# Kernel tuning notes

Measured on AMD Instinct MI355X. Metric: run time of the kernel, lower is better.

## Reference

```python
import jax, jax.numpy as jnp
import numpy as np

KH, KW, STRIDE, PAD, DIL = 3, 3, 1, 1, 1


def setup_inputs() -> dict:
    key = jax.random.key(0)
    k1, k2, k3, k4, k5 = jax.random.split(key, 5)
    B, Cin, H, W = 8, 64, 128, 128
    Cout = 64
    K = KH * KW
    Ho = (H + 2 * PAD - DIL * (KH - 1) - 1) // STRIDE + 1
    Wo = (W + 2 * PAD - DIL * (KW - 1) - 1) // STRIDE + 1
    return {
        "input": jax.random.normal(k1, (B, Cin, H, W), dtype=jnp.float32),
        "offset": jax.random.normal(k2, (B, 2 * K, Ho, Wo), dtype=jnp.float32),
        "mask": jax.random.uniform(k3, (B, K, Ho, Wo), dtype=jnp.float32),
        "weight": jax.random.normal(k4, (Cout, Cin, KH, KW), dtype=jnp.float32) * 0.05,
        "bias": jax.random.normal(k5, (Cout,), dtype=jnp.float32) * 0.01,
    }


def _bilinear_gather(xb, py, px):
    # xb: [C,H,W]; py/px: [K,Ho,Wo] fractional sample coords. Zero padding outside.
    C, H, W = xb.shape
    y0 = jnp.floor(py)
    x0 = jnp.floor(px)
    wy = py - y0
    wx = px - x0

    def g(yi, xi):
        yi = yi.astype(jnp.int32)
        xi = xi.astype(jnp.int32)
        valid = ((yi >= 0) & (yi < H) & (xi >= 0) & (xi < W)).astype(xb.dtype)
        yc = jnp.clip(yi, 0, H - 1)
        xc = jnp.clip(xi, 0, W - 1)
        return xb[:, yc, xc] * valid[None]  # [C,K,Ho,Wo]

    return (g(y0, x0) * ((1 - wy) * (1 - wx))[None]
            + g(y0, x0 + 1) * ((1 - wy) * wx)[None]
            + g(y0 + 1, x0) * (wy * (1 - wx))[None]
            + g(y0 + 1, x0 + 1) * (wy * wx)[None])


def _deform_conv2d(x, offset, mask, weight, bias):
    B, Cin, H, W = x.shape
    Cout = weight.shape[0]
    K = KH * KW
    _, _, Ho, Wo = mask.shape
    # base sampling grid per kernel tap
    kh = jnp.arange(KH)
    kw = jnp.arange(KW)
    base_y = (jnp.arange(Ho) * STRIDE - PAD)[None, :] + (kh * DIL)[:, None]  # [KH,Ho]
    base_x = (jnp.arange(Wo) * STRIDE - PAD)[None, :] + (kw * DIL)[:, None]  # [KW,Wo]
    base_y = jnp.repeat(base_y, KW, axis=0)              # [K,Ho]
    base_x = jnp.tile(base_x, (KH, 1))                   # [K,Wo]
    off = offset.reshape(B, K, 2, Ho, Wo)                # torchvision layout: (y,x) per tap
    py = base_y[None, :, :, None].astype(x.dtype) + off[:, :, 0]  # [B,K,Ho,Wo]
    px = base_x[None, :, None, :].astype(x.dtype) + off[:, :, 1]
    sampled = jax.vmap(_bilinear_gather)(x, py, px)      # [B,Cin,K,Ho,Wo]
    sampled = sampled * mask[:, None]                    # modulated (DCNv2)
    w = weight.reshape(Cout, Cin, K)
    out = jnp.einsum('bckhw,ock->bohw', sampled, w) + bias[None, :, None, None]
    return out


def reference(input, offset, mask, weight, bias):
    out = _deform_conv2d(input, offset, mask, weight, bias)
    return jnp.clip(out, 0.0, 6.0)  # ReLU6
```

## Files before the change

### kernel.cpp

```cpp
#include <hip/hip_runtime.h>

typedef __attribute__((ext_vector_type(8))) short short8;
typedef __attribute__((ext_vector_type(8))) unsigned short ushort8;
typedef __attribute__((ext_vector_type(4))) float floatx4;
typedef __attribute__((ext_vector_type(4))) unsigned int uintx4;

constexpr int B = 8, Cin = 64, Hh = 128, Ww = 128, Cout = 64, Kt = 9, Ho = 128, Wo = 128;

__device__ __forceinline__ unsigned short f2bf(float f) {
    unsigned int u = __float_as_uint(f);
    unsigned int r = (u + 0x7fffu + ((u >> 16) & 1u)) >> 16;
    return (unsigned short)r;
}

__device__ __forceinline__ unsigned int cvtpk(float lo, float hi) {
    unsigned int r;
    asm("v_cvt_pk_bf16_f32 %0, %1, %2" : "=v"(r) : "v"(lo), "v"(hi));
    return r;
}
__device__ __forceinline__ float dot2bf(unsigned int a, unsigned int b, float c) {
    float d;
    asm("v_dot2_f32_bf16 %0, %1, %2, %3" : "=v"(d) : "v"(a), "v"(b), "v"(c));
    return d;
}

__global__ void prep_w(const float* __restrict__ w, unsigned short* __restrict__ wA) {
    int i = blockIdx.x * 256 + threadIdx.x;
    if (i >= Cout * Cin * Kt) return;
    int o = i / (Cin * Kt);
    int r = i % (Cin * Kt);
    int c = r / Kt;
    int k = r % Kt;
    wA[o * 576 + k * 64 + c] = f2bf(w[i]);
}

__global__ __launch_bounds__(256) void to_nhwc(const float* __restrict__ in,
                                               unsigned short* __restrict__ xn) {
    __shared__ float s[64 * 65];
    const int t = threadIdx.x;
    const int blk = blockIdx.x;
    const int b = blk >> 8;
    const int y = (blk & 255) >> 1;
    const int x0 = (blk & 1) * 64;
    const float* src = in + ((size_t)(b * 64) * 128 + y) * 128 + x0;
    #pragma unroll
    for (int i = 0; i < 16; ++i) {
        int c = i * 4 + (t >> 6);
        s[c * 65 + (t & 63)] = src[(size_t)c * 16384 + (t & 63)];
    }
    __syncthreads();
    const int x = t >> 2, c0 = (t & 3) * 16;
    ushort8 o0, o1;
    #pragma unroll
    for (int j = 0; j < 8; ++j) {
        o0[j] = f2bf(s[(c0 + j) * 65 + x]);
        o1[j] = f2bf(s[(c0 + 8 + j) * 65 + x]);
    }
    unsigned short* dst = xn + (((size_t)(b * 128 + y) * 128 + x0 + x) * 64 + c0);
    *(ushort8*)dst = o0;
    *(ushort8*)(dst + 8) = o1;
}

__global__ __launch_bounds__(256) void dcn_mfma(
    const unsigned short* __restrict__ xn, const float* __restrict__ off,
    const float* __restrict__ msk, const unsigned short* __restrict__ wA,
    const float* __restrict__ bias, float* __restrict__ out) {
    __shared__ uintx4 s_meta[Kt * 64];
    __shared__ unsigned short s_b[64 * 64];

    const int t = threadIdx.x;
    int blk = blockIdx.x;
    blk = (blk & 7) * 256 + (blk >> 3);
    const int b = blk >> 8;
    const int ho = (blk & 255) >> 1;
    const int w0 = (blk & 1) * 64;

    const int wv = t >> 6;
    const int l = t & 63;
    const int p = t >> 2;
    const int cg = t & 3;

    for (int idx = t; idx < Kt * 64; idx += 256) {
        const int k = idx >> 6, pp = idx & 63;
        const int kh = k / 3, kw = k - kh * 3;
        const int wo = w0 + pp;
        const size_t obase = ((size_t)b * 18 + 2 * k) * 16384 + ho * 128 + wo;
        const float oy = off[obase];
        const float ox = off[obase + 16384];
        const float m = msk[((size_t)b * 9 + k) * 16384 + ho * 128 + wo];
        const float py = (float)(ho - 1 + kh) + oy;
        const float px = (float)(wo - 1 + kw) + ox;
        const float y0f = floorf(py), x0f = floorf(px);
        const int iy0 = (int)y0f, ix0 = (int)x0f;
        const float wy = py - y0f, wx = px - x0f;
        const int iy1 = iy0 + 1, ix1 = ix0 + 1;
        const bool vy0 = ((unsigned)iy0 < 128u), vy1 = ((unsigned)iy1 < 128u);
        const bool vx0 = ((unsigned)ix0 < 128u), vx1 = ((unsigned)ix1 < 128u);
        const float w00 = (1.f - wy) * (1.f - wx) * m * ((vy0 && vx0) ? 1.f : 0.f);
        const float w01 = (1.f - wy) * wx * m * ((vy0 && vx1) ? 1.f : 0.f);
        const float w10 = wy * (1.f - wx) * m * ((vy1 && vx0) ? 1.f : 0.f);
        const float w11 = wy * wx * m * ((vy1 && vx1) ? 1.f : 0.f);
        const int cy0 = min(max(iy0, 0), 127), cy1 = min(max(iy1, 0), 127);
        const int cx0 = min(max(ix0, 0), 127), cx1 = min(max(ix1, 0), 127);
        const unsigned o00 = (unsigned)(cy0 * 128 + cx0), o01 = (unsigned)(cy0 * 128 + cx1);
        const unsigned o10 = (unsigned)(cy1 * 128 + cx0), o11 = (unsigned)(cy1 * 128 + cx1);
        uintx4 mt;
        mt.x = cvtpk(w00, w01);
        mt.y = cvtpk(w10, w11);
        mt.z = o00 | (o01 << 16);
        mt.w = o10 | (o11 << 16);
        s_meta[idx] = mt;
    }
    __syncthreads();

    floatx4 acc[4] = {};

    const unsigned short* wbase = wA + (16 * wv + (l & 15)) * 576 + (l >> 4) * 8;
    const unsigned short* xb = xn + (size_t)b * (128 * 128 * 64) + cg * 16;
    const int ckA = (cg * 2) ^ (p & 7);
    const int ckB = (cg * 2 + 1) ^ (p & 7);
    unsigned short* wrA = &s_b[p * 64 + ckA * 8];
    unsigned short* wrB = &s_b[p * 64 + ckB * 8];
    int rdo[8];
    #pragma unroll
    for (int h = 0; h < 2; ++h)
        #pragma unroll
        for (int f = 0; f < 4; ++f) {
            const int pp = 16 * f + (l & 15);
            const int ck = (h * 4 + (l >> 4)) ^ (pp & 7);
            rdo[h * 4 + f] = pp * 64 + ck * 8;
        }

    for (int k = 0; k < Kt; ++k) {
        const short8 a0 = *(const short8*)(wbase + k * 64);
        const short8 a1 = *(const short8*)(wbase + k * 64 + 32);

        const uintx4 mt = s_meta[k * 64 + p];
        const unsigned wp01 = mt.x, wp23 = mt.y;
        const uintx4* c00 = (const uintx4*)(xb + ((size_t)(mt.z & 0xffffu) << 6));
        const uintx4* c01 = (const uintx4*)(xb + ((size_t)(mt.z >> 16) << 6));
        const uintx4* c10 = (const uintx4*)(xb + ((size_t)(mt.w & 0xffffu) << 6));
        const uintx4* c11 = (const uintx4*)(xb + ((size_t)(mt.w >> 16) << 6));
        const uintx4 q00a = c00[0], q00b = c00[1];
        const uintx4 q01a = c01[0], q01b = c01[1];
        const uintx4 q10a = c10[0], q10b = c10[1];
        const uintx4 q11a = c11[0], q11b = c11[1];

        uintx4 vA, vB;
        #pragma unroll
        for (int j = 0; j < 4; ++j) {
            const unsigned pa = __builtin_amdgcn_perm(q01a[j], q00a[j], 0x05040100u);
            const unsigned pb = __builtin_amdgcn_perm(q11a[j], q10a[j], 0x05040100u);
            const unsigned pc = __builtin_amdgcn_perm(q01a[j], q00a[j], 0x07060302u);
            const unsigned pd = __builtin_amdgcn_perm(q11a[j], q10a[j], 0x07060302u);
            const float f0 = dot2bf(pa, wp01, dot2bf(pb, wp23, 0.f));
            const float f1 = dot2bf(pc, wp01, dot2bf(pd, wp23, 0.f));
            vA[j] = cvtpk(f0, f1);
        }
        #pragma unroll
        for (int j = 0; j < 4; ++j) {
            const unsigned pa = __builtin_amdgcn_perm(q01b[j], q00b[j], 0x05040100u);
            const unsigned pb = __builtin_amdgcn_perm(q11b[j], q10b[j], 0x05040100u);
            const unsigned pc = __builtin_amdgcn_perm(q01b[j], q00b[j], 0x07060302u);
            const unsigned pd = __builtin_amdgcn_perm(q11b[j], q10b[j], 0x07060302u);
            const float f0 = dot2bf(pa, wp01, dot2bf(pb, wp23, 0.f));
            const float f1 = dot2bf(pc, wp01, dot2bf(pd, wp23, 0.f));
            vB[j] = cvtpk(f0, f1);
        }
        *(uintx4*)wrA = vA;
        *(uintx4*)wrB = vB;
        __syncthreads();

        #pragma unroll
        for (int h = 0; h < 2; ++h) {
            const short8 a = h ? a1 : a0;
            #pragma unroll
            for (int f = 0; f < 4; ++f) {
                const short8 bfrag = *(const short8*)&s_b[rdo[h * 4 + f]];
                acc[f] = __builtin_amdgcn_mfma_f32_16x16x32_bf16(a, bfrag, acc[f], 0, 0, 0);
            }
        }
        __syncthreads();
    }

    #pragma unroll
    for (int f = 0; f < 4; ++f) {
        #pragma unroll
        for (int r = 0; r < 4; ++r) {
            const int co = 16 * wv + (l >> 4) * 4 + r;
            float v = acc[f][r] + bias[co];
            v = fminf(fmaxf(v, 0.f), 6.f);
            out[(((size_t)b * 64 + co) * 128 + ho) * 128 + w0 + 16 * f + (l & 15)] = v;
        }
    }
}

constexpr int NT = 64;
constexpr int LDSS = 68;

__global__ void reorder_weight(const float* __restrict__ w, float* __restrict__ wT) {
    int i = blockIdx.x * blockDim.x + threadIdx.x;
    if (i >= Cout * Cin * Kt) return;
    int o = i / (Cin * Kt);
    int r = i % (Cin * Kt);
    int c = r / Kt;
    int k = r % Kt;
    wT[(k * Cin + c) * Cout + o] = w[i];
}

__global__ __launch_bounds__(256, 4) void dcn_kernel(
    const float* __restrict__ in, const float* __restrict__ off,
    const float* __restrict__ msk, const float* __restrict__ wT,
    const float* __restrict__ bias, float* __restrict__ out) {
    __shared__ float s_w[Cin * LDSS];
    __shared__ float s_s[Cin * LDSS];
    const int tid = threadIdx.x;
    const int blk = blockIdx.x;
    const int b = blk >> 8;
    const int ho = (blk & 255) >> 1;
    const int w0 = (blk & 1) * NT;
    const int lane = tid & 63;
    const int c4 = tid >> 6;
    const int ty = tid >> 4;
    const int tx = tid & 15;
    const float* in_b = in + b * (Cin * Hh * Ww);
    const int wo = w0 + lane;
    float acc[4][4];
    #pragma unroll
    for (int i = 0; i < 4; ++i)
        #pragma unroll
        for (int j = 0; j < 4; ++j) acc[i][j] = 0.f;
    for (int k = 0; k < Kt; ++k) {
        {
            const float* src = wT + k * (Cin * Cout);
            const int c = tid >> 2;
            const int g = tid & 3;
            const float4* s = (const float4*)(src + c * Cout + g * 16);
            float4* dq = (float4*)(&s_w[c * LDSS + g * 16]);
            dq[0] = s[0]; dq[1] = s[1]; dq[2] = s[2]; dq[3] = s[3];
        }
        {
            const int kh = k / 3, kw = k % 3;
            const float oy = off[(((size_t)b * 2 * Kt + 2 * k) * Ho + ho) * Wo + wo];
            const float ox = off[(((size_t)b * 2 * Kt + 2 * k + 1) * Ho + ho) * Wo + wo];
            const float m = msk[(((size_t)b * Kt + k) * Ho + ho) * Wo + wo];
            const float py = (float)(ho - 1 + kh) + oy;
            const float px = (float)(wo - 1 + kw) + ox;
            const float y0f = floorf(py), x0f = floorf(px);
            const int iy0 = (int)y0f, ix0 = (int)x0f;
            const float wy = py - y0f, wx = px - x0f;
            const int iy1 = iy0 + 1, ix1 = ix0 + 1;
            const bool vy0 = (iy0 >= 0) & (iy0 < Hh);
            const bool vy1 = (iy1 >= 0) & (iy1 < Hh);
            const bool vx0 = (ix0 >= 0) & (ix0 < Ww);
            const bool vx1 = (ix1 >= 0) & (ix1 < Ww);
            const int cy0 = min(max(iy0, 0), Hh - 1), cy1 = min(max(iy1, 0), Hh - 1);
            const int cx0 = min(max(ix0, 0), Ww - 1), cx1 = min(max(ix1, 0), Ww - 1);
            const float w00 = (1.f - wy) * (1.f - wx) * m * ((vy0 & vx0) ? 1.f : 0.f);
            const float w01 = (1.f - wy) * wx * m * ((vy0 & vx1) ? 1.f : 0.f);
            const float w10 = wy * (1.f - wx) * m * ((vy1 & vx0) ? 1.f : 0.f);
            const float w11 = wy * wx * m * ((vy1 & vx1) ? 1.f : 0.f);
            const int o00 = cy0 * Ww + cx0, o01 = cy0 * Ww + cx1;
            const int o10 = cy1 * Ww + cx0, o11 = cy1 * Ww + cx1;
            const float* pp = in_b + (c4 * 16) * (Hh * Ww);
            #pragma unroll
            for (int ii = 0; ii < 16; ++ii) {
                float v = pp[o00] * w00 + pp[o01] * w01 + pp[o10] * w10 + pp[o11] * w11;
                s_s[(c4 * 16 + ii) * LDSS + lane] = v;
                pp += Hh * Ww;
            }
        }
        __syncthreads();
        #pragma unroll 8
        for (int c = 0; c < Cin; ++c) {
            const float4 a = *(const float4*)(&s_w[c * LDSS + ty * 4]);
            const float4 bv = *(const float4*)(&s_s[c * LDSS + tx * 4]);
            const float* ap = (const float*)&a;
            const float* bp = (const float*)&bv;
            #pragma unroll
            for (int i = 0; i < 4; ++i)
                #pragma unroll
                for (int j = 0; j < 4; ++j) acc[i][j] += ap[i] * bp[j];
        }
        __syncthreads();
    }
    #pragma unroll
    for (int i = 0; i < 4; ++i) {
        const int co = ty * 4 + i;
        const float bs = bias[co];
        float4 r;
        float* rp = (float*)&r;
        #pragma unroll
        for (int j = 0; j < 4; ++j) {
            float v = acc[i][j] + bs;
            v = fminf(fmaxf(v, 0.f), 6.f);
            rp[j] = v;
        }
        *(float4*)(&out[(((size_t)b * Cout + co) * Ho + ho) * Wo + w0 + tx * 4]) = r;
    }
}

extern "C" void kernel_launch(void* const* d_in, const int* in_sizes, int n_in,
                              void* d_out, int out_size, void* d_ws, size_t ws_size,
                              hipStream_t stream) {
    const float* in = (const float*)d_in[0];
    const float* off = (const float*)d_in[1];
    const float* msk = (const float*)d_in[2];
    const float* w = (const float*)d_in[3];
    const float* bias = (const float*)d_in[4];
    float* out = (float*)d_out;

    const size_t needX = (size_t)8 * 128 * 128 * 64 * 2;
    const size_t xoff = 131072;
    if (ws_size >= xoff + needX) {
        unsigned short* wAb = (unsigned short*)d_ws;
        unsigned short* xnb = (unsigned short*)((char*)d_ws + xoff);
        prep_w<<<144, 256, 0, stream>>>(w, wAb);
        to_nhwc<<<2048, 256, 0, stream>>>(in, xnb);
        dcn_mfma<<<2048, 256, 0, stream>>>(xnb, off, msk, wAb, bias, out);
    } else {
        float* wT = (float*)d_ws;
        reorder_weight<<<(Cout * Cin * Kt + 255) / 256, 256, 0, stream>>>(w, wT);
        dcn_kernel<<<(B * Ho * Wo) / NT, 256, 0, stream>>>(in, off, msk, wT, bias, out);
    }
}
```

Measured before the change: 61.14 us.

## Process two taps per iteration with double-buffered LDS to batch gathers

The tap loop now issues the bilinear gathers for two kernel taps back to back, blends both into two separate LDS buffers, then runs the MFMAs for both taps after a single barrier. This halves the number of barrier pairs and puts more global loads in flight at once, hiding gather latency. Address math is also switched to 32-bit byte offsets. The cost is roughly doubled live gather registers, which may lower occupancy, plus a larger LDS footprint.

```diff
diff --git a/kernel.cpp b/kernel.cpp
--- a/kernel.cpp
+++ b/kernel.cpp
@@ -12,7 +12,6 @@
     unsigned int r = (u + 0x7fffu + ((u >> 16) & 1u)) >> 16;
     return (unsigned short)r;
 }
-
 __device__ __forceinline__ unsigned int cvtpk(float lo, float hi) {
     unsigned int r;
     asm("v_cvt_pk_bf16_f32 %0, %1, %2" : "=v"(r) : "v"(lo), "v"(hi));
@@ -61,12 +60,17 @@
     *(ushort8*)(dst + 8) = o1;
 }
 
+struct Gath {
+    uintx4 q0, q1, q2, q3, q4, q5, q6, q7;
+    unsigned wp01, wp23;
+};
+
 __global__ __launch_bounds__(256) void dcn_mfma(
     const unsigned short* __restrict__ xn, const float* __restrict__ off,
     const float* __restrict__ msk, const unsigned short* __restrict__ wA,
     const float* __restrict__ bias, float* __restrict__ out) {
     __shared__ uintx4 s_meta[Kt * 64];
-    __shared__ unsigned short s_b[64 * 64];
+    __shared__ unsigned short s_b[2][64 * 64];
 
     const int t = threadIdx.x;
     int blk = blockIdx.x;
@@ -111,16 +115,16 @@
         mt.w = o10 | (o11 << 16);
         s_meta[idx] = mt;
     }
-    __syncthreads();
 
     floatx4 acc[4] = {};
 
     const unsigned short* wbase = wA + (16 * wv + (l & 15)) * 576 + (l >> 4) * 8;
-    const unsigned short* xb = xn + (size_t)b * (128 * 128 * 64) + cg * 16;
+    const char* xbase = (const char*)(xn + (size_t)b * (128 * 128 * 64));
+    const unsigned cgb = (unsigned)cg * 32u;
     const int ckA = (cg * 2) ^ (p & 7);
     const int ckB = (cg * 2 + 1) ^ (p & 7);
-    unsigned short* wrA = &s_b[p * 64 + ckA * 8];
-    unsigned short* wrB = &s_b[p * 64 + ckB * 8];
+    const int wrA = p * 64 + ckA * 8;
+    const int wrB = p * 64 + ckB * 8;
     int rdo[8];
     #pragma unroll
     for (int h = 0; h < 2; ++h)
@@ -131,56 +135,78 @@
             rdo[h * 4 + f] = pp * 64 + ck * 8;
         }
 
-    for (int k = 0; k < Kt; ++k) {
+    __syncthreads();
+
+    auto issue = [&](int k) -> Gath {
+        Gath g;
+        const uintx4 mt = s_meta[k * 64 + p];
+        g.wp01 = mt.x;
+        g.wp23 = mt.y;
+        const unsigned f00 = ((mt.z & 0xffffu) << 7) + cgb;
+        const unsigned f01 = ((mt.z >> 16) << 7) + cgb;
+        const unsigned f10 = ((mt.w & 0xffffu) << 7) + cgb;
+        const unsigned f11 = ((mt.w >> 16) << 7) + cgb;
+        const uintx4* c00 = (const uintx4*)(xbase + f00);
+        const uintx4* c01 = (const uintx4*)(xbase + f01);
+        const uintx4* c10 = (const uintx4*)(xbase + f10);
+        const uintx4* c11 = (const uintx4*)(xbase + f11);
+        g.q0 = c00[0]; g.q1 = c00[1];
+        g.q2 = c01[0]; g.q3 = c01[1];
+        g.q4 = c10[0]; g.q5 = c10[1];
+        g.q6 = c11[0]; g.q7 = c11[1];
+        return g;
+    };
+    auto blend_write = [&](int slot, const Gath& g) {
+        uintx4 vA, vB;
+        #pragma unroll
+        for (int j = 0; j < 4; ++j) {
+            const unsigned pa = __builtin_amdgcn_perm(g.q2[j], g.q0[j], 0x05040100u);
+            const unsigned pb = __builtin_amdgcn_perm(g.q6[j], g.q4[j], 0x05040100u);
+            const unsigned pc = __builtin_amdgcn_perm(g.q2[j], g.q0[j], 0x07060302u);
+            const unsigned pd = __builtin_amdgcn_perm(g.q6[j], g.q4[j], 0x07060302u);
+            const float f0 = dot2bf(pa, g.wp01, dot2bf(pb, g.wp23, 0.f));
+            const float f1 = dot2bf(pc, g.wp01, dot2bf(pd, g.wp23, 0.f));
+            vA[j] = cvtpk(f0, f1);
+        }
+        #pragma unroll
+        for (int j = 0; j < 4; ++j) {
+            const unsigned pa = __builtin_amdgcn_perm(g.q3[j], g.q1[j], 0x05040100u);
+            const unsigned pb = __builtin_amdgcn_perm(g.q7[j], g.q5[j], 0x05040100u);
+            const unsigned pc = __builtin_amdgcn_perm(g.q3[j], g.q1[j], 0x07060302u);
+            const unsigned pd = __builtin_amdgcn_perm(g.q7[j], g.q5[j], 0x07060302u);
+            const float f0 = dot2bf(pa, g.wp01, dot2bf(pb, g.wp23, 0.f));
+            const float f1 = dot2bf(pc, g.wp01, dot2bf(pd, g.wp23, 0.f));
+            vB[j] = cvtpk(f0, f1);
+        }
+        *(uintx4*)&s_b[slot][wrA] = vA;
+        *(uintx4*)&s_b[slot][wrB] = vB;
+    };
+    auto mfma_tap = [&](int slot, int k) {
         const short8 a0 = *(const short8*)(wbase + k * 64);
         const short8 a1 = *(const short8*)(wbase + k * 64 + 32);
-
-        const uintx4 mt = s_meta[k * 64 + p];
-        const unsigned wp01 = mt.x, wp23 = mt.y;
-        const uintx4* c00 = (const uintx4*)(xb + ((size_t)(mt.z & 0xffffu) << 6));
-        const uintx4* c01 = (const uintx4*)(xb + ((size_t)(mt.z >> 16) << 6));
-        const uintx4* c10 = (const uintx4*)(xb + ((size_t)(mt.w & 0xffffu) << 6));
-        const uintx4* c11 = (const uintx4*)(xb + ((size_t)(mt.w >> 16) << 6));
-        const uintx4 q00a = c00[0], q00b = c00[1];
-        const uintx4 q01a = c01[0], q01b = c01[1];
-        const uintx4 q10a = c10[0], q10b = c10[1];
-        const uintx4 q11a = c11[0], q11b = c11[1];
-
-        uintx4 vA, vB;
-        #pragma unroll
-        for (int j = 0; j < 4; ++j) {
-            const unsigned pa = __builtin_amdgcn_perm(q01a[j], q00a[j], 0x05040100u);
-            const unsigned pb = __builtin_amdgcn_perm(q11a[j], q10a[j], 0x05040100u);
-            const unsigned pc = __builtin_amdgcn_perm(q01a[j], q00a[j], 0x07060302u);
-            const unsigned pd = __builtin_amdgcn_perm(q11a[j], q10a[j], 0x07060302u);
-            const float f0 = dot2bf(pa, wp01, dot2bf(pb, wp23, 0.f));
-            const float f1 = dot2bf(pc, wp01, dot2bf(pd, wp23, 0.f));
-            vA[j] = cvtpk(f0, f1);
-        }
-        #pragma unroll
-        for (int j = 0; j < 4; ++j) {
-            const unsigned pa = __builtin_amdgcn_perm(q01b[j], q00b[j], 0x05040100u);
-            const unsigned pb = __builtin_amdgcn_perm(q11b[j], q10b[j], 0x05040100u);
-            const unsigned pc = __builtin_amdgcn_perm(q01b[j], q00b[j], 0x07060302u);
-            const unsigned pd = __builtin_amdgcn_perm(q11b[j], q10b[j], 0x07060302u);
-            const float f0 = dot2bf(pa, wp01, dot2bf(pb, wp23, 0.f));
-            const float f1 = dot2bf(pc, wp01, dot2bf(pd, wp23, 0.f));
-            vB[j] = cvtpk(f0, f1);
-        }
-        *(uintx4*)wrA = vA;
-        *(uintx4*)wrB = vB;
-        __syncthreads();
-
         #pragma unroll
         for (int h = 0; h < 2; ++h) {
             const short8 a = h ? a1 : a0;
             #pragma unroll
             for (int f = 0; f < 4; ++f) {
-                const short8 bfrag = *(const short8*)&s_b[rdo[h * 4 + f]];
+                const short8 bfrag = *(const short8*)&s_b[slot][rdo[h * 4 + f]];
                 acc[f] = __builtin_amdgcn_mfma_f32_16x16x32_bf16(a, bfrag, acc[f], 0, 0, 0);
             }
         }
+    };
+
+    for (int j = 0; j < 5; ++j) {
+        const int k0 = 2 * j;
+        const bool has2 = (k0 + 1 < Kt);
+        Gath ga = issue(k0);
+        Gath gb;
+        if (has2) gb = issue(k0 + 1);
+        blend_write(0, ga);
+        if (has2) blend_write(1, gb);
         __syncthreads();
+        mfma_tap(0, k0);
+        if (has2) mfma_tap(1, k0 + 1);
+        if (j < 4) __syncthreads();
     }
 
     #pragma unroll
```

Result: no change. 60.91 us, median of 2 (-0.4%).

## Feed bilinear samples directly into MFMA B fragments, removing the LDS staging

Applied to the files above, without the earlier changes.

The bilinear-interpolated activations are now produced in registers in exactly the MFMA B-operand layout. Each wave owns 16 output pixels and computes all 64 output channels, so the shared-memory staging buffer and the two per-tap __syncthreads are gone. The weights are pre-swizzled into a per-lane fragment layout, so each lane loads eight contiguous short8 A fragments per tap. The trade-off is more global/L2 weight traffic per wave (the full weight tile instead of a 16-row slice), and launch bounds now request 4 blocks per CU.

```diff
diff --git a/kernel.cpp b/kernel.cpp
--- a/kernel.cpp
+++ b/kernel.cpp
@@ -12,7 +12,6 @@
     unsigned int r = (u + 0x7fffu + ((u >> 16) & 1u)) >> 16;
     return (unsigned short)r;
 }
-
 __device__ __forceinline__ unsigned int cvtpk(float lo, float hi) {
     unsigned int r;
     asm("v_cvt_pk_bf16_f32 %0, %1, %2" : "=v"(r) : "v"(lo), "v"(hi));
@@ -24,14 +23,17 @@
     return d;
 }
 
-__global__ void prep_w(const float* __restrict__ w, unsigned short* __restrict__ wA) {
+__global__ void prep_w(const float* __restrict__ w, unsigned short* __restrict__ wA2) {
     int i = blockIdx.x * 256 + threadIdx.x;
     if (i >= Cout * Cin * Kt) return;
     int o = i / (Cin * Kt);
     int r = i % (Cin * Kt);
     int c = r / Kt;
     int k = r % Kt;
-    wA[o * 576 + k * 64 + c] = f2bf(w[i]);
+    const int h = c >> 5, sub = (c >> 3) & 3, j = c & 7;
+    const int l = sub * 16 + (o & 15);
+    const int g = o >> 4;
+    wA2[(size_t)(((k * 2 + h) * 4 + g) * 64 + l) * 8 + j] = f2bf(w[i]);
 }
 
 __global__ __launch_bounds__(256) void to_nhwc(const float* __restrict__ in,
@@ -61,12 +63,11 @@
     *(ushort8*)(dst + 8) = o1;
 }
 
-__global__ __launch_bounds__(256) void dcn_mfma(
+__global__ __launch_bounds__(256, 4) void dcn_mfma(
     const unsigned short* __restrict__ xn, const float* __restrict__ off,
-    const float* __restrict__ msk, const unsigned short* __restrict__ wA,
+    const float* __restrict__ msk, const unsigned short* __restrict__ wA2,
     const float* __restrict__ bias, float* __restrict__ out) {
     __shared__ uintx4 s_meta[Kt * 64];
-    __shared__ unsigned short s_b[64 * 64];
 
     const int t = threadIdx.x;
     int blk = blockIdx.x;
@@ -77,8 +78,6 @@
 
     const int wv = t >> 6;
     const int l = t & 63;
-    const int p = t >> 2;
-    const int cg = t & 3;
 
     for (int idx = t; idx < Kt * 64; idx += 256) {
         const int k = idx >> 6, pp = idx & 63;
@@ -115,82 +114,69 @@
 
     floatx4 acc[4] = {};
 
-    const unsigned short* wbase = wA + (16 * wv + (l & 15)) * 576 + (l >> 4) * 8;
-    const unsigned short* xb = xn + (size_t)b * (128 * 128 * 64) + cg * 16;
-    const int ckA = (cg * 2) ^ (p & 7);
-    const int ckB = (cg * 2 + 1) ^ (p & 7);
-    unsigned short* wrA = &s_b[p * 64 + ckA * 8];
-    unsigned short* wrB = &s_b[p * 64 + ckB * 8];
-    int rdo[8];
-    #pragma unroll
-    for (int h = 0; h < 2; ++h)
-        #pragma unroll
-        for (int f = 0; f < 4; ++f) {
-            const int pp = 16 * f + (l & 15);
-            const int ck = (h * 4 + (l >> 4)) ^ (pp & 7);
-            rdo[h * 4 + f] = pp * 64 + ck * 8;
-        }
-
+    const char* xbase = (const char*)(xn + (size_t)b * (128 * 128 * 64));
+    const unsigned chb = ((unsigned)(l >> 4)) * 16u;
+    const uintx4* mbase = &s_meta[wv * 16 + (l & 15)];
+    const unsigned short* abase = wA2 + (size_t)l * 8;
+
+    #pragma unroll 1
     for (int k = 0; k < Kt; ++k) {
-        const short8 a0 = *(const short8*)(wbase + k * 64);
-        const short8 a1 = *(const short8*)(wbase + k * 64 + 32);
-
-        const uintx4 mt = s_meta[k * 64 + p];
+        const uintx4 mt = mbase[k * 64];
         const unsigned wp01 = mt.x, wp23 = mt.y;
-        const uintx4* c00 = (const uintx4*)(xb + ((size_t)(mt.z & 0xffffu) << 6));
-        const uintx4* c01 = (const uintx4*)(xb + ((size_t)(mt.z >> 16) << 6));
-        const uintx4* c10 = (const uintx4*)(xb + ((size_t)(mt.w & 0xffffu) << 6));
-        const uintx4* c11 = (const uintx4*)(xb + ((size_t)(mt.w >> 16) << 6));
-        const uintx4 q00a = c00[0], q00b = c00[1];
-        const uintx4 q01a = c01[0], q01b = c01[1];
-        const uintx4 q10a = c10[0], q10b = c10[1];
-        const uintx4 q11a = c11[0], q11b = c11[1];
-
-        uintx4 vA, vB;
+        const unsigned f00 = ((mt.z & 0xffffu) << 7) + chb;
+        const unsigned f01 = ((mt.z >> 16) << 7) + chb;
+        const unsigned f10 = ((mt.w & 0xffffu) << 7) + chb;
+        const unsigned f11 = ((mt.w >> 16) << 7) + chb;
+        const uintx4 q00l = *(const uintx4*)(xbase + f00);
+        const uintx4 q00h = *(const uintx4*)(xbase + f00 + 64);
+        const uintx4 q01l = *(const uintx4*)(xbase + f01);
+        const uintx4 q01h = *(const uintx4*)(xbase + f01 + 64);
+        const uintx4 q10l = *(const uintx4*)(xbase + f10);
+        const uintx4 q10h = *(const uintx4*)(xbase + f10 + 64);
+        const uintx4 q11l = *(const uintx4*)(xbase + f11);
+        const uintx4 q11h = *(const uintx4*)(xbase + f11 + 64);
+        const unsigned short* ak = abase + k * 4096;
+        short8 a[8];
+        #pragma unroll
+        for (int i = 0; i < 8; ++i) a[i] = *(const short8*)(ak + i * 512);
+        uintx4 v0, v1;
         #pragma unroll
         for (int j = 0; j < 4; ++j) {
-            const unsigned pa = __builtin_amdgcn_perm(q01a[j], q00a[j], 0x05040100u);
-            const unsigned pb = __builtin_amdgcn_perm(q11a[j], q10a[j], 0x05040100u);
-            const unsigned pc = __builtin_amdgcn_perm(q01a[j], q00a[j], 0x07060302u);
-            const unsigned pd = __builtin_amdgcn_perm(q11a[j], q10a[j], 0x07060302u);
+            const unsigned pa = __builtin_amdgcn_perm(q01l[j], q00l[j], 0x05040100u);
+            const unsigned pb = __builtin_amdgcn_perm(q11l[j], q10l[j], 0x05040100u);
+            const unsigned pc = __builtin_amdgcn_perm(q01l[j], q00l[j], 0x07060302u);
+            const unsigned pd = __builtin_amdgcn_perm(q11l[j], q10l[j], 0x07060302u);
             const float f0 = dot2bf(pa, wp01, dot2bf(pb, wp23, 0.f));
             const float f1 = dot2bf(pc, wp01, dot2bf(pd, wp23, 0.f));
-            vA[j] = cvtpk(f0, f1);
+            v0[j] = cvtpk(f0, f1);
         }
         #pragma unroll
         for (int j = 0; j < 4; ++j) {
-            const unsigned pa = __builtin_amdgcn_perm(q01b[j], q00b[j], 0x05040100u);
-            const unsigned pb = __builtin_amdgcn_perm(q11b[j], q10b[j], 0x05040100u);
-            const unsigned pc = __builtin_amdgcn_perm(q01b[j], q00b[j], 0x07060302u);
-            const unsigned pd = __builtin_amdgcn_perm(q11b[j], q10b[j], 0x07060302u);
+            const unsigned pa = __builtin_amdgcn_perm(q01h[j], q00h[j], 0x05040100u);
+            const unsigned pb = __builtin_amdgcn_perm(q11h[j], q10h[j], 0x05040100u);
+            const unsigned pc = __builtin_amdgcn_perm(q01h[j], q00h[j], 0x07060302u);
+            const unsigned pd = __builtin_amdgcn_perm(q11h[j], q10h[j], 0x07060302u);
             const float f0 = dot2bf(pa, wp01, dot2bf(pb, wp23, 0.f));
             const float f1 = dot2bf(pc, wp01, dot2bf(pd, wp23, 0.f));
-            vB[j] = cvtpk(f0, f1);
-        }
-        *(uintx4*)wrA = vA;
-        *(uintx4*)wrB = vB;
-        __syncthreads();
-
-        #pragma unroll
-        for (int h = 0; h < 2; ++h) {
-            const short8 a = h ? a1 : a0;
-            #pragma unroll
-            for (int f = 0; f < 4; ++f) {
-                const short8 bfrag = *(const short8*)&s_b[rdo[h * 4 + f]];
-                acc[f] = __builtin_amdgcn_mfma_f32_16x16x32_bf16(a, bfrag, acc[f], 0, 0, 0);
-            }
-        }
-        __syncthreads();
-    }
-
-    #pragma unroll
-    for (int f = 0; f < 4; ++f) {
+            v1[j] = cvtpk(f0, f1);
+        }
+        const short8 b0 = *(const short8*)&v0;
+        const short8 b1 = *(const short8*)&v1;
+        #pragma unroll
+        for (int g = 0; g < 4; ++g) {
+            acc[g] = __builtin_amdgcn_mfma_f32_16x16x32_bf16(a[g], b0, acc[g], 0, 0, 0);
+            acc[g] = __builtin_amdgcn_mfma_f32_16x16x32_bf16(a[4 + g], b1, acc[g], 0, 0, 0);
+        }
+    }
+
+    #pragma unroll
+    for (int g = 0; g < 4; ++g) {
         #pragma unroll
         for (int r = 0; r < 4; ++r) {
-            const int co = 16 * wv + (l >> 4) * 4 + r;
-            float v = acc[f][r] + bias[co];
+            const int co = g * 16 + (l >> 4) * 4 + r;
+            float v = acc[g][r] + bias[co];
             v = fminf(fmaxf(v, 0.f), 6.f);
-            out[(((size_t)b * 64 + co) * 128 + ho) * 128 + w0 + 16 * f + (l & 15)] = v;
+            out[(((size_t)b * 64 + co) * 128 + ho) * 128 + w0 + wv * 16 + (l & 15)] = v;
         }
     }
 }
```

Result: slower. 110.6 us (+80.8%).
